# Kernel tuning notes

Measured on AMD Instinct MI355X. Metric: run time of the kernel, lower is better.

The kernel has to match this reference:

```python
import jax, jax.numpy as jnp
import numpy as np

D_MODEL, N_HEADS, D_FF, CTX_DIM = 512, 8, 2048, 20
D_K = D_MODEL // N_HEADS
SCALE = float(np.sqrt(D_K))
EPS = 1e-5


def _ln(x, g, b):
    mu = jnp.mean(x, axis=-1, keepdims=True)
    var = jnp.mean((x - mu) ** 2, axis=-1, keepdims=True)
    return (x - mu) * jax.lax.rsqrt(var + EPS) * g + b


def setup_inputs() -> dict:
    key = jax.random.key(0)
    ks = jax.random.split(key, 20)
    B, S = 2, 2048
    s = lambda d: 1.0 / np.sqrt(d)
    return {
        "x": jax.random.normal(ks[0], (B, S, D_MODEL), jnp.float32),
        "context": jax.random.normal(ks[1], (B, CTX_DIM), jnp.float32),
        "wq": jax.random.normal(ks[2], (D_MODEL, D_MODEL), jnp.float32) * s(D_MODEL),
        "wk": jax.random.normal(ks[3], (D_MODEL, D_MODEL), jnp.float32) * s(D_MODEL),
        "wv": jax.random.normal(ks[4], (D_MODEL, D_MODEL), jnp.float32) * s(D_MODEL),
        "wo": jax.random.normal(ks[5], (D_MODEL, D_MODEL), jnp.float32) * s(D_MODEL),
        "wo_b": jnp.zeros((D_MODEL,), jnp.float32),
        "wc": jax.random.normal(ks[6], (CTX_DIM, D_MODEL), jnp.float32) * s(CTX_DIM),
        "wc_b": jnp.zeros((D_MODEL,), jnp.float32),
        "wg": jax.random.normal(ks[7], (2 * D_MODEL, D_MODEL), jnp.float32) * s(2 * D_MODEL),
        "wg_b": jnp.zeros((D_MODEL,), jnp.float32),
        "opt_bias": jnp.zeros((N_HEADS, 1, 1), jnp.float32),
        "w1": jax.random.normal(ks[8], (D_MODEL, D_FF), jnp.float32) * s(D_MODEL),
        "b1": jnp.zeros((D_FF,), jnp.float32),
        "w2": jax.random.normal(ks[9], (D_FF, D_MODEL), jnp.float32) * s(D_FF),
        "b2": jnp.zeros((D_MODEL,), jnp.float32),
        "g1": jnp.ones((D_MODEL,), jnp.float32),
        "be1": jnp.zeros((D_MODEL,), jnp.float32),
        "g2": jnp.ones((D_MODEL,), jnp.float32),
        "be2": jnp.zeros((D_MODEL,), jnp.float32),
    }


def reference(x, context, wq, wk, wv, wo, wo_b, wc, wc_b, wg, wg_b, opt_bias,
              w1, b1, w2, b2, g1, be1, g2, be2):
    B, S, _ = x.shape
    # QKV projections -> [B, H, S, d_k]
    Q = (x @ wq).reshape(B, S, N_HEADS, D_K).transpose(0, 2, 1, 3)
    K = (x @ wk).reshape(B, S, N_HEADS, D_K).transpose(0, 2, 1, 3)
    V = (x @ wv).reshape(B, S, N_HEADS, D_K).transpose(0, 2, 1, 3)
    # scores [B, H, S, S] + learned per-head bias
    scores = jnp.einsum('bhqd,bhkd->bhqk', Q, K) / SCALE + opt_bias[None]
    # context-gated second score term
    ctx_proj = context @ wc + wc_b                      # [B, d_model]
    ctx_exp = jnp.broadcast_to(ctx_proj[:, None, :], (B, S, D_MODEL))
    combined = jnp.concatenate([x, ctx_exp], axis=-1)   # [B, S, 2*d_model]
    gate = jax.nn.sigmoid(combined @ wg + wg_b)         # [B, S, d_model]
    ctx_h = ctx_proj.reshape(B, N_HEADS, D_K)           # per-head context vectors
    ci = jnp.einsum('bhsd,bhd->bhs', Q, ctx_h) / SCALE  # [B, H, S]
    gate_h = gate.reshape(B, S, N_HEADS, D_K).mean(-1).transpose(0, 2, 1)  # [B, H, S]
    scores = scores + (ci * gate_h)[..., None]          # broadcast over keys
    attn = jax.nn.softmax(scores, axis=-1)
    ctx_out = jnp.einsum('bhqk,bhkd->bhqd', attn, V)
    ctx_out = ctx_out.transpose(0, 2, 1, 3).reshape(B, S, D_MODEL)
    attn_out = ctx_out @ wo + wo_b
    # residual + LN, FFN (exact GELU), residual + LN
    h = _ln(x + attn_out, g1, be1)
    ff = jax.nn.gelu(h @ w1 + b1, approximate=False) @ w2 + b2
    return _ln(h + ff, g2, be2)
```

## Files before the change

### kernel.cpp

```cpp
#include <hip/hip_runtime.h>
#include <hip/hip_bf16.h>
#include <math.h>

#define D_MODEL 512
#define N_HEADS 8
#define D_K     64
#define D_FF    2048
#define B_      2
#define S_      2048
#define M_TOT   (B_ * S_)
#define NSPLIT  4

#define QSCALE  0.18033688011112042f

typedef __attribute__((ext_vector_type(8))) __bf16 bf16x8;
typedef __attribute__((ext_vector_type(4))) __bf16 bf16x4;
typedef __attribute__((ext_vector_type(4))) float  f32x4;
typedef __attribute__((ext_vector_type(4))) unsigned int u32x4;

static __device__ inline f32x4 mfma16(bf16x8 a, bf16x8 b, f32x4 c) {
    return __builtin_amdgcn_mfma_f32_16x16x32_bf16(a, b, c, 0, 0, 0);
}

static __device__ inline void gld_lds16(const __bf16* g, __bf16* l) {
    __builtin_amdgcn_global_load_lds(
        (const __attribute__((address_space(1))) void*)g,
        (__attribute__((address_space(3))) void*)l, 16, 0, 0);
}

static __device__ inline unsigned int pack_bf16(float a, float b) {
    union { __bf16 h; unsigned short u; } ua, ub;
    ua.h = (__bf16)a; ub.h = (__bf16)b;
    return (unsigned int)ua.u | ((unsigned int)ub.u << 16);
}

__global__ __launch_bounds__(256) void k_prep(const float* __restrict__ x,
                                              const float* __restrict__ wq,
                                              const float* __restrict__ wk,
                                              const float* __restrict__ wv,
                                              const float* __restrict__ wo,
                                              const float* __restrict__ w1,
                                              const float* __restrict__ w2,
                                              __bf16* __restrict__ xb,
                                              __bf16* __restrict__ wqkvT,
                                              __bf16* __restrict__ woT,
                                              __bf16* __restrict__ w1T,
                                              __bf16* __restrict__ w2T) {
    int bid = blockIdx.x, tid = threadIdx.x;
    if (bid < 2048) {
        int i = (bid * 256 + tid) * 4;
        float4 f = *(const float4*)(x + i);
        bf16x4 o = { (__bf16)f.x, (__bf16)f.y, (__bf16)f.z, (__bf16)f.w };
        *(bf16x4*)(xb + i) = o;
        return;
    }
    __shared__ __bf16 t64[64 * 72];
    int tt = bid - 2048;
    const float* W; __bf16* WT; int N, K, ntiles, local;
    if (tt < 256) {
        N = 512; K = 512; ntiles = 8;
        if (tt < 64)       { W = wq; WT = wqkvT;          local = tt; }
        else if (tt < 128) { W = wk; WT = wqkvT + 262144; local = tt - 64; }
        else if (tt < 192) { W = wv; WT = wqkvT + 524288; local = tt - 128; }
        else               { W = wo; WT = woT;            local = tt - 192; }
    } else if (tt < 512)   { W = w1; WT = w1T; N = 2048; K = 512;  ntiles = 32; local = tt - 256; }
    else                   { W = w2; WT = w2T; N = 512;  K = 2048; ntiles = 8;  local = tt - 512; }
    int k0 = (local / ntiles) * 64, n0 = (local % ntiles) * 64;

#pragma unroll
    for (int it = 0; it < 4; it++) {
        int i = it * 256 + tid;
        int r = i >> 4, c4 = i & 15;
        float4 v = ((const float4*)(W + (size_t)(k0 + r) * N + n0))[c4];
        t64[(c4 * 4 + 0) * 72 + r] = (__bf16)v.x;
        t64[(c4 * 4 + 1) * 72 + r] = (__bf16)v.y;
        t64[(c4 * 4 + 2) * 72 + r] = (__bf16)v.z;
        t64[(c4 * 4 + 3) * 72 + r] = (__bf16)v.w;
    }
    __syncthreads();
#pragma unroll
    for (int it = 0; it < 2; it++) {
        int j = it * 256 + tid;
        int n = j >> 3, c8 = j & 7;
        bf16x8 v = *(const bf16x8*)&t64[n * 72 + c8 * 8];
        *(bf16x8*)&WT[(size_t)(n0 + n) * K + k0 + c8 * 8] = v;
    }
}

template<int BN, int MODE>
__global__ __launch_bounds__(256) void k_gemm128(const __bf16* __restrict__ A,
                                                 const __bf16* __restrict__ BT,
                                                 const float* __restrict__ bias,
                                                 void* __restrict__ out,
                                                 int M, int N, int K) {
    __shared__ __bf16 lds[(128 + BN) * 64];
    const int tid = threadIdx.x;
    const int lane = tid & 63, w = tid >> 6;
    const int lr = lane & 15, hi = lane >> 4;
    const int wm = w >> 1, wn = w & 1;
    const int bm0 = blockIdx.y * 128, bn0 = blockIdx.x * BN;
    constexpr int NT  = BN / 32;
    constexpr int BIT = BN / 32;
    f32x4 acc[4][NT] = {};

    for (int kt = 0; kt < K; kt += 64) {
#pragma unroll
        for (int a = 0; a < 4; a++) {
            int idx16 = a * 256 + tid;
            int r = idx16 >> 3, c8 = idx16 & 7;
            int k8 = c8 ^ (r & 7);
            gld_lds16(A + (size_t)(bm0 + r) * K + kt + k8 * 8,
                      (__bf16*)lds + (size_t)(a * 256 + w * 64) * 8);
        }
#pragma unroll
        for (int bq = 0; bq < BIT; bq++) {
            int idx16 = bq * 256 + tid;
            int r = idx16 >> 3, c8 = idx16 & 7;
            int k8 = c8 ^ (r & 7);
            gld_lds16(BT + (size_t)(bn0 + r) * K + kt + k8 * 8,
                      (__bf16*)lds + 128 * 64 + (size_t)(bq * 256 + w * 64) * 8);
        }
        __syncthreads();
#pragma unroll
        for (int kc = 0; kc < 2; kc++) {
            bf16x8 af[4], bf[NT];
#pragma unroll
            for (int mt = 0; mt < 4; mt++) {
                int r = wm * 64 + mt * 16 + lr;
                int c8 = (kc * 4 + hi) ^ (r & 7);
                af[mt] = *(const bf16x8*)&lds[r * 64 + c8 * 8];
            }
#pragma unroll
            for (int nt = 0; nt < NT; nt++) {
                int r = wn * (BN / 2) + nt * 16 + lr;
                int c8 = (kc * 4 + hi) ^ (r & 7);
                bf[nt] = *(const bf16x8*)&lds[128 * 64 + r * 64 + c8 * 8];
            }
#pragma unroll
            for (int mt = 0; mt < 4; mt++)
#pragma unroll
                for (int nt = 0; nt < NT; nt++)
                    acc[mt][nt] = mfma16(af[mt], bf[nt], acc[mt][nt]);
        }
        __syncthreads();
    }

#pragma unroll
    for (int mt = 0; mt < 4; mt++)
#pragma unroll
    for (int nt = 0; nt < NT; nt++)
#pragma unroll
    for (int i = 0; i < 4; i++) {
        int m = bm0 + wm * 64 + mt * 16 + hi * 4 + i;
        int n = bn0 + wn * (BN / 2) + nt * 16 + lr;
        float v = acc[mt][nt][i];
        if constexpr (MODE == 0) {
            int b = m >> 11, s = m & 2047;
            int seg = n >> 9, nn = n & 511;
            int h = nn >> 6, d = nn & 63;
            __bf16* base = (__bf16*)out;
            if (seg == 0)
                base[(((size_t)(b * N_HEADS + h)) * S_ + s) * D_K + d] = (__bf16)(v * QSCALE);
            else if (seg == 1)
                base[2097152 + (((size_t)(b * N_HEADS + h)) * S_ + s) * D_K + d] = (__bf16)v;
            else
                base[4194304 + (((size_t)(b * N_HEADS + h)) * D_K + d) * S_ + s] = (__bf16)v;
        } else if constexpr (MODE == 2) {
            v += bias[n];
            float gg = 0.5f * v * (1.0f + erff(v * 0.70710678118654752f));
            ((__bf16*)out)[(size_t)m * N + n] = (__bf16)gg;
        } else {
            ((float*)out)[(size_t)m * N + n] = v + bias[n];
        }
    }
}

__global__ __launch_bounds__(256, 8) void k_attn2(const __bf16* __restrict__ Q,
                                                  const __bf16* __restrict__ Kq,
                                                  const __bf16* __restrict__ VT,
                                                  float* __restrict__ pO,
                                                  float* __restrict__ pm,
                                                  float* __restrict__ pl) {
    const int lane = threadIdx.x & 63;
    const int w    = threadIdx.x >> 6;
    const int bh   = blockIdx.y;
    const int sp   = blockIdx.z;
    const int q0   = blockIdx.x * 64 + w * 16;
    const int lr   = lane & 15;
    const int hi   = lane >> 4;

    const __bf16* Qp = Q  + (size_t)bh * S_ * D_K;
    const __bf16* Kp = Kq + (size_t)bh * S_ * D_K;
    const __bf16* Vp = VT + (size_t)bh * D_K * S_;

    bf16x8 bq0 = *(const bf16x8*)&Qp[(size_t)(q0 + lr) * D_K + hi * 8];
    bf16x8 bq1 = *(const bf16x8*)&Qp[(size_t)(q0 + lr) * D_K + 32 + hi * 8];

    f32x4 acc[4] = {};
    float mrun = -1e30f, lrun = 0.0f;
    const int src0 = lr + ((hi & 1) << 5);
    const int src1 = src0 + 16;
    const bool csel = (hi & 2) != 0;

    const int j0 = sp * (S_ / NSPLIT);
    for (int j = j0; j < j0 + S_ / NSPLIT; j += 64) {
        f32x4 sc[4] = {};
        __builtin_amdgcn_s_setprio(1);
#pragma unroll
        for (int c = 0; c < 4; c++) {
            bf16x8 ak0 = *(const bf16x8*)&Kp[(size_t)(j + c * 16 + lr) * D_K + hi * 8];
            bf16x8 ak1 = *(const bf16x8*)&Kp[(size_t)(j + c * 16 + lr) * D_K + 32 + hi * 8];
            sc[c] = mfma16(ak0, bq0, sc[c]);
            sc[c] = mfma16(ak1, bq1, sc[c]);
        }
        __builtin_amdgcn_s_setprio(0);
        float mt0 = fmaxf(fmaxf(sc[0][0], sc[0][1]), fmaxf(sc[0][2], sc[0][3]));
        float mt1 = fmaxf(fmaxf(sc[1][0], sc[1][1]), fmaxf(sc[1][2], sc[1][3]));
        float mt2 = fmaxf(fmaxf(sc[2][0], sc[2][1]), fmaxf(sc[2][2], sc[2][3]));
        float mt3 = fmaxf(fmaxf(sc[3][0], sc[3][1]), fmaxf(sc[3][2], sc[3][3]));
        float mt = fmaxf(fmaxf(mt0, mt1), fmaxf(mt2, mt3));
        mt = fmaxf(mt, __shfl_xor(mt, 16));
        mt = fmaxf(mt, __shfl_xor(mt, 32));
        float mnew = fmaxf(mrun, mt);
        float scl = exp2f(mrun - mnew);
        mrun = mnew;
        float p[4][4];
        float ps = 0.0f;
#pragma unroll
        for (int c = 0; c < 4; c++)
#pragma unroll
            for (int i = 0; i < 4; i++) {
                p[c][i] = exp2f(sc[c][i] - mnew);
                ps += p[c][i];
            }
        ps += __shfl_xor(ps, 16);
        ps += __shfl_xor(ps, 32);
        lrun = lrun * scl + ps;
        unsigned int pk[4][2];
#pragma unroll
        for (int c = 0; c < 4; c++) {
            pk[c][0] = pack_bf16(p[c][0], p[c][1]);
            pk[c][1] = pack_bf16(p[c][2], p[c][3]);
        }
        bf16x8 pb[2];
#pragma unroll
        for (int t = 0; t < 2; t++) {
            unsigned int d0a = __shfl((int)pk[2 * t][0],     src0);
            unsigned int d0b = __shfl((int)pk[2 * t + 1][0], src0);
            unsigned int d1a = __shfl((int)pk[2 * t][1],     src0);
            unsigned int d1b = __shfl((int)pk[2 * t + 1][1], src0);
            unsigned int d2a = __shfl((int)pk[2 * t][0],     src1);
            unsigned int d2b = __shfl((int)pk[2 * t + 1][0], src1);
            unsigned int d3a = __shfl((int)pk[2 * t][1],     src1);
            unsigned int d3b = __shfl((int)pk[2 * t + 1][1], src1);
            u32x4 u = { csel ? d0b : d0a, csel ? d1b : d1a,
                        csel ? d2b : d2a, csel ? d3b : d3a };
            pb[t] = __builtin_bit_cast(bf16x8, u);
        }
#pragma unroll
        for (int dt = 0; dt < 4; dt++)
#pragma unroll
            for (int i = 0; i < 4; i++) acc[dt][i] *= scl;
        __builtin_amdgcn_s_setprio(1);
#pragma unroll
        for (int dt = 0; dt < 4; dt++) {
            bf16x8 va0 = *(const bf16x8*)&Vp[(size_t)(dt * 16 + lr) * S_ + j + hi * 8];
            bf16x8 va1 = *(const bf16x8*)&Vp[(size_t)(dt * 16 + lr) * S_ + j + 32 + hi * 8];
            acc[dt] = mfma16(va0, pb[0], acc[dt]);
            acc[dt] = mfma16(va1, pb[1], acc[dt]);
        }
        __builtin_amdgcn_s_setprio(0);
    }

    float* pOw = pO + ((size_t)(sp * 16 + bh) * S_ + (q0 + lr)) * D_K;
#pragma unroll
    for (int dt = 0; dt < 4; dt++)
        *(f32x4*)&pOw[dt * 16 + hi * 4] = acc[dt];
    if (hi == 0) {
        int idx = (sp * 16 + bh) * S_ + q0 + lr;
        pm[idx] = mrun;
        pl[idx] = lrun;
    }
}

__global__ __launch_bounds__(256) void k_comb(const float* __restrict__ pO,
                                              const float* __restrict__ pm,
                                              const float* __restrict__ pl,
                                              __bf16* __restrict__ ctx) {
    int tid = threadIdx.x;
    int d = tid & 63, r4 = tid >> 6;
    int q = blockIdx.x * 4 + r4, bh = blockIdx.y;
    float m[NSPLIT], l[NSPLIT];
#pragma unroll
    for (int sp = 0; sp < NSPLIT; sp++) {
        int idx = (sp * 16 + bh) * S_ + q;
        m[sp] = pm[idx];
        l[sp] = pl[idx];
    }
    float ms = m[0];
#pragma unroll
    for (int sp = 1; sp < NSPLIT; sp++) ms = fmaxf(ms, m[sp]);
    float ls = 0.0f, o = 0.0f;
#pragma unroll
    for (int sp = 0; sp < NSPLIT; sp++) {
        float wsp = exp2f(m[sp] - ms);
        ls += wsp * l[sp];
        o  += wsp * pO[((size_t)(sp * 16 + bh) * S_ + q) * D_K + d];
    }
    int b = bh >> 3, h = bh & 7;
    ctx[((size_t)(b * S_ + q)) * D_MODEL + h * D_K + d] = (__bf16)(o / ls);
}

template<int WRITE_BF16>
__global__ __launch_bounds__(256) void k_ln(const float* __restrict__ base,
                                            const float* __restrict__ delta,
                                            const float* __restrict__ g,
                                            const float* __restrict__ be,
                                            float* __restrict__ outf,
                                            __bf16* __restrict__ outb) {
    int row  = blockIdx.x * 4 + (threadIdx.x >> 6);
    int lane = threadIdx.x & 63;
    const float4* A  = (const float4*)(base  + (size_t)row * D_MODEL);
    const float4* Bv = (const float4*)(delta + (size_t)row * D_MODEL);
    float4 a0 = A[lane],  a1 = A[lane + 64];
    float4 b0 = Bv[lane], b1 = Bv[lane + 64];
    float v[8] = { a0.x + b0.x, a0.y + b0.y, a0.z + b0.z, a0.w + b0.w,
                   a1.x + b1.x, a1.y + b1.y, a1.z + b1.z, a1.w + b1.w };
    float s1 = 0.0f, s2 = 0.0f;
#pragma unroll
    for (int j = 0; j < 8; j++) { s1 += v[j]; s2 += v[j] * v[j]; }
#pragma unroll
    for (int m = 1; m <= 32; m <<= 1) {
        s1 += __shfl_xor(s1, m);
        s2 += __shfl_xor(s2, m);
    }
    float mean = s1 * (1.0f / D_MODEL);
    float var  = s2 * (1.0f / D_MODEL) - mean * mean;
    float rstd = rsqrtf(var + 1e-5f);
    const float4* G  = (const float4*)g;
    const float4* Be = (const float4*)be;
    float4 g0 = G[lane],  g1v = G[lane + 64];
    float4 e0 = Be[lane], e1  = Be[lane + 64];
    float y[8];
    y[0] = (v[0] - mean) * rstd * g0.x  + e0.x;
    y[1] = (v[1] - mean) * rstd * g0.y  + e0.y;
    y[2] = (v[2] - mean) * rstd * g0.z  + e0.z;
    y[3] = (v[3] - mean) * rstd * g0.w  + e0.w;
    y[4] = (v[4] - mean) * rstd * g1v.x + e1.x;
    y[5] = (v[5] - mean) * rstd * g1v.y + e1.y;
    y[6] = (v[6] - mean) * rstd * g1v.z + e1.z;
    y[7] = (v[7] - mean) * rstd * g1v.w + e1.w;
    float4* O = (float4*)(outf + (size_t)row * D_MODEL);
    O[lane]      = make_float4(y[0], y[1], y[2], y[3]);
    O[lane + 64] = make_float4(y[4], y[5], y[6], y[7]);
    if constexpr (WRITE_BF16) {
        bf16x4 o0 = { (__bf16)y[0], (__bf16)y[1], (__bf16)y[2], (__bf16)y[3] };
        bf16x4 o1 = { (__bf16)y[4], (__bf16)y[5], (__bf16)y[6], (__bf16)y[7] };
        *(bf16x4*)&outb[(size_t)row * D_MODEL + lane * 4]       = o0;
        *(bf16x4*)&outb[(size_t)row * D_MODEL + 256 + lane * 4] = o1;
    }
}

extern "C" void kernel_launch(void* const* d_in, const int* in_sizes, int n_in,
                              void* d_out, int out_size, void* d_ws, size_t ws_size,
                              hipStream_t stream) {
    const float* x    = (const float*)d_in[0];
    const float* wq   = (const float*)d_in[2];
    const float* wk   = (const float*)d_in[3];
    const float* wv   = (const float*)d_in[4];
    const float* wo   = (const float*)d_in[5];
    const float* wo_b = (const float*)d_in[6];
    const float* w1   = (const float*)d_in[12];
    const float* b1   = (const float*)d_in[13];
    const float* w2   = (const float*)d_in[14];
    const float* b2   = (const float*)d_in[15];
    const float* g1   = (const float*)d_in[16];
    const float* be1  = (const float*)d_in[17];
    const float* g2   = (const float*)d_in[18];
    const float* be2  = (const float*)d_in[19];
    float* out = (float*)d_out;

    char* ws = (char*)d_ws;
    size_t off = 0;
    auto alloc = [&](size_t bytes) {
        void* p = ws + off;
        off += (bytes + 255) & ~(size_t)255;
        return p;
    };
    __bf16* xb    = (__bf16*)alloc((size_t)M_TOT * D_MODEL * 2);
    __bf16* wqkvT = (__bf16*)alloc((size_t)3 * D_MODEL * D_MODEL * 2);
    __bf16* woT   = (__bf16*)alloc((size_t)D_MODEL * D_MODEL * 2);
    __bf16* w1T   = (__bf16*)alloc((size_t)D_MODEL * D_FF * 2);
    __bf16* w2T   = (__bf16*)alloc((size_t)D_FF * D_MODEL * 2);
    __bf16* qkv   = (__bf16*)alloc((size_t)3 * M_TOT * D_MODEL * 2);
    __bf16* ctx   = (__bf16*)alloc((size_t)M_TOT * D_MODEL * 2);
    float*  aout  = (float*)alloc((size_t)M_TOT * D_MODEL * 4);
    float*  hf    = (float*)alloc((size_t)M_TOT * D_MODEL * 4);
    __bf16* hb    = (__bf16*)alloc((size_t)M_TOT * D_MODEL * 2);
    __bf16* ffb   = (__bf16*)alloc((size_t)M_TOT * D_FF * 2);
    float*  ff2   = (float*)alloc((size_t)M_TOT * D_MODEL * 4);
    float*  pO    = (float*)alloc((size_t)NSPLIT * 16 * S_ * D_K * 4);
    float*  pm    = (float*)alloc((size_t)NSPLIT * 16 * S_ * 4);
    float*  pl    = (float*)alloc((size_t)NSPLIT * 16 * S_ * 4);
    (void)ws_size; (void)in_sizes; (void)n_in; (void)out_size;

    __bf16* Qb  = qkv;
    __bf16* Kb  = qkv + (size_t)M_TOT * D_MODEL;
    __bf16* VTb = qkv + (size_t)2 * M_TOT * D_MODEL;

    dim3 blk(256);
    k_prep<<<dim3(2048 + 768), blk, 0, stream>>>(x, wq, wk, wv, wo, w1, w2,
                                                 xb, wqkvT, woT, w1T, w2T);
    k_gemm128<128, 0><<<dim3(12, 32), blk, 0, stream>>>(xb, wqkvT, nullptr, qkv,
                                                        M_TOT, 3 * D_MODEL, D_MODEL);
    k_attn2<<<dim3(S_ / 64, B_ * N_HEADS, NSPLIT), blk, 0, stream>>>(Qb, Kb, VTb,
                                                                     pO, pm, pl);
    k_comb<<<dim3(S_ / 4, B_ * N_HEADS), blk, 0, stream>>>(pO, pm, pl, ctx);
    k_gemm128<64, 1><<<dim3(8, 32), blk, 0, stream>>>(ctx, woT, wo_b, aout,
                                                      M_TOT, D_MODEL, D_MODEL);
    k_ln<1><<<dim3(M_TOT / 4), blk, 0, stream>>>(x, aout, g1, be1, hf, hb);
    k_gemm128<128, 2><<<dim3(16, 32), blk, 0, stream>>>(hb, w1T, b1, ffb,
                                                        M_TOT, D_FF, D_MODEL);
    k_gemm128<64, 3><<<dim3(8, 32), blk, 0, stream>>>(ffb, w2T, b2, ff2,
                                                      M_TOT, D_MODEL, D_FF);
    k_ln<0><<<dim3(M_TOT / 4), blk, 0, stream>>>(hf, ff2, g2, be2, out, nullptr);
}
```

Before: 339.7 us.

## Stage K and V tiles in swizzled LDS shared across attention waves

The attention kernel now cooperatively loads each 64-key K tile and V^T tile into LDS using direct global-to-LDS copies with an XOR swizzle, and the four waves read their MFMA operands from LDS. Before, each wave fetched K and V separately from global memory. The aim is to cut redundant global/L2 traffic four-fold and avoid bank conflicts. In exchange it adds two barriers and a full vmcnt wait per tile with no double buffering, so load latency is no longer overlapped with compute.

```diff
diff --git a/kernel.cpp b/kernel.cpp
--- a/kernel.cpp
+++ b/kernel.cpp
@@ -181,8 +181,11 @@
                                                   float* __restrict__ pO,
                                                   float* __restrict__ pm,
                                                   float* __restrict__ pl) {
-    const int lane = threadIdx.x & 63;
-    const int w    = threadIdx.x >> 6;
+    __shared__ __bf16 Kl[64 * 64];
+    __shared__ __bf16 Vl[64 * 64];
+    const int tid  = threadIdx.x;
+    const int lane = tid & 63;
+    const int w    = tid >> 6;
     const int bh   = blockIdx.y;
     const int sp   = blockIdx.z;
     const int q0   = blockIdx.x * 64 + w * 16;
@@ -204,16 +207,32 @@
 
     const int j0 = sp * (S_ / NSPLIT);
     for (int j = j0; j < j0 + S_ / NSPLIT; j += 64) {
+        __syncthreads();
+#pragma unroll
+        for (int it = 0; it < 2; it++) {
+            int idx16 = it * 256 + tid;
+            int r = idx16 >> 3, c8 = idx16 & 7;
+            int k8 = c8 ^ (r & 7);
+            gld_lds16(Kp + (size_t)(j + r) * D_K + k8 * 8,
+                      Kl + (size_t)(it * 256 + w * 64) * 8);
+            gld_lds16(Vp + (size_t)r * S_ + j + k8 * 8,
+                      Vl + (size_t)(it * 256 + w * 64) * 8);
+        }
+        asm volatile("s_waitcnt vmcnt(0)" ::: "memory");
+        __syncthreads();
+
         f32x4 sc[4] = {};
         __builtin_amdgcn_s_setprio(1);
 #pragma unroll
         for (int c = 0; c < 4; c++) {
-            bf16x8 ak0 = *(const bf16x8*)&Kp[(size_t)(j + c * 16 + lr) * D_K + hi * 8];
-            bf16x8 ak1 = *(const bf16x8*)&Kp[(size_t)(j + c * 16 + lr) * D_K + 32 + hi * 8];
+            int r = c * 16 + lr;
+            bf16x8 ak0 = *(const bf16x8*)&Kl[r * 64 + (hi ^ (r & 7)) * 8];
+            bf16x8 ak1 = *(const bf16x8*)&Kl[r * 64 + ((4 + hi) ^ (r & 7)) * 8];
             sc[c] = mfma16(ak0, bq0, sc[c]);
             sc[c] = mfma16(ak1, bq1, sc[c]);
         }
         __builtin_amdgcn_s_setprio(0);
+
         float mt0 = fmaxf(fmaxf(sc[0][0], sc[0][1]), fmaxf(sc[0][2], sc[0][3]));
         float mt1 = fmaxf(fmaxf(sc[1][0], sc[1][1]), fmaxf(sc[1][2], sc[1][3]));
         float mt2 = fmaxf(fmaxf(sc[2][0], sc[2][1]), fmaxf(sc[2][2], sc[2][3]));
@@ -261,11 +280,13 @@
         for (int dt = 0; dt < 4; dt++)
 #pragma unroll
             for (int i = 0; i < 4; i++) acc[dt][i] *= scl;
+
         __builtin_amdgcn_s_setprio(1);
 #pragma unroll
         for (int dt = 0; dt < 4; dt++) {
-            bf16x8 va0 = *(const bf16x8*)&Vp[(size_t)(dt * 16 + lr) * S_ + j + hi * 8];
-            bf16x8 va1 = *(const bf16x8*)&Vp[(size_t)(dt * 16 + lr) * S_ + j + 32 + hi * 8];
+            int r = dt * 16 + lr;
+            bf16x8 va0 = *(const bf16x8*)&Vl[r * 64 + (hi ^ (r & 7)) * 8];
+            bf16x8 va1 = *(const bf16x8*)&Vl[r * 64 + ((4 + hi) ^ (r & 7)) * 8];
             acc[dt] = mfma16(va0, pb[0], acc[dt]);
             acc[dt] = mfma16(va1, pb[1], acc[dt]);
         }
```

Result: faster. 278.2 us (-18.1%).
